# Kernel optimization log

Hardware: AMD Instinct MI355X
Metric: run time of the kernel (lower is better)

## Reference

```python
import jax, jax.numpy as jnp
import numpy as np

ISO = 0.0
DIM = 64
# MC corner numbering: 0..7 around the cube, main diagonal corner0=(0,0,0) -> corner6=(1,1,1)
OFF = [(0,0,0),(1,0,0),(1,1,0),(0,1,0),(0,0,1),(1,0,1),(1,1,1),(0,1,1)]
# 6-tetrahedra decomposition of a voxel around the 0-6 diagonal
TETS = np.array([[0,1,2,6],[0,2,3,6],[0,3,7,6],[0,7,4,6],[0,4,5,6],[0,5,1,6]], dtype=np.int32)
# tet edges: e0=(0,1) e1=(0,2) e2=(0,3) e3=(1,2) e4=(1,3) e5=(2,3)
EDGE_A = np.array([0,0,0,1,1,2], dtype=np.int32)
EDGE_B = np.array([1,2,3,2,3,3], dtype=np.int32)
# marching-tetrahedra case table: case = bitmask of (value > iso) per tet corner;
# each row lists up to 2 triangles as tet-edge ids, -1 = unused slot
TRI_TABLE = np.array([
    [-1,-1,-1,-1,-1,-1],
    [ 0, 1, 2,-1,-1,-1],
    [ 0, 4, 3,-1,-1,-1],
    [ 1, 2, 4, 1, 4, 3],
    [ 1, 3, 5,-1,-1,-1],
    [ 0, 3, 5, 0, 5, 2],
    [ 0, 4, 5, 0, 5, 1],
    [ 2, 4, 5,-1,-1,-1],
    [ 2, 5, 4,-1,-1,-1],
    [ 0, 5, 4, 0, 1, 5],
    [ 0, 5, 3, 0, 2, 5],
    [ 1, 5, 3,-1,-1,-1],
    [ 1, 4, 2, 1, 3, 4],
    [ 0, 3, 4,-1,-1,-1],
    [ 0, 2, 1,-1,-1,-1],
    [-1,-1,-1,-1,-1,-1]], dtype=np.int32)


def _mc(grid, deform, iso):
    X, Y, Z = grid.shape
    # pad scalar field with iso+1 (outside), deform with 0 -- mirrors DiffMC.forward
    Gp = jnp.pad(grid, 1, constant_values=iso + 1.0)
    Dp = jnp.pad(deform, ((1,1),(1,1),(1,1),(0,0)))
    ax = [jnp.arange(s, dtype=grid.dtype) for s in (X+2, Y+2, Z+2)]
    coords = jnp.stack(jnp.meshgrid(*ax, indexing='ij'), axis=-1)  # [X+2,Y+2,Z+2,3]
    P = coords + Dp                                                 # deformed grid-point positions
    Vx, Vy, Vz = X+1, Y+1, Z+1                                      # number of voxels per axis
    Vc = jnp.stack([Gp[dx:dx+Vx, dy:dy+Vy, dz:dz+Vz] for dx,dy,dz in OFF], axis=-1).reshape(-1, 8)
    Pc = jnp.stack([P[dx:dx+Vx, dy:dy+Vy, dz:dz+Vz] for dx,dy,dz in OFF], axis=-2).reshape(-1, 8, 3)
    tv = Vc[:, TETS].reshape(-1, 4)        # [M,4] tet corner values, M = 6*Vx*Vy*Vz
    tp = Pc[:, TETS].reshape(-1, 4, 3)     # [M,4,3] tet corner positions
    M = tv.shape[0]
    code = ((tv > iso).astype(jnp.int32) * jnp.array([1, 2, 4, 8], dtype=jnp.int32)).sum(-1)
    tri = jnp.asarray(TRI_TABLE)[code]     # [M,6] edge ids (2 triangle slots)
    valid = tri >= 0
    e = jnp.where(valid, tri, 0)
    a = jnp.asarray(EDGE_A)[e]
    b = jnp.asarray(EDGE_B)[e]
    va = jnp.take_along_axis(tv, a, axis=1)
    vb = jnp.take_along_axis(tv, b, axis=1)
    a3 = jnp.broadcast_to(a[:, :, None], (M, 6, 3))
    b3 = jnp.broadcast_to(b[:, :, None], (M, 6, 3))
    pa = jnp.take_along_axis(tp, a3, axis=1)
    pb = jnp.take_along_axis(tp, b3, axis=1)
    den = vb - va
    t = (iso - va) / jnp.where(jnp.abs(den) > 1e-8, den, 1.0)
    t = jnp.clip(t, 0.0, 1.0)[..., None]
    pos = pa + t * (pb - pa)               # edge-interpolated surface vertices [M,6,3]
    scale = jnp.array([X-1, Y-1, Z-1], dtype=grid.dtype)
    verts = ((pos - 1.0) / scale) * valid[..., None].astype(grid.dtype)  # undo pad, normalize to [0,1]
    verts = verts.reshape(-1, 3, 3)        # [2*M triangles, 3 corners, xyz]
    mask = valid.reshape(-1, 3)[:, 0]      # triangle validity (all 3 slots set together)
    return verts, mask


def setup_inputs() -> dict:
    key = jax.random.key(0)
    k1, k2 = jax.random.split(key)
    grid = jax.random.normal(k1, (DIM, DIM, DIM), dtype=jnp.float32)
    deform = 0.3 * jax.random.normal(k2, (DIM, DIM, DIM, 3), dtype=jnp.float32)
    return {"grid": grid, "deform": deform}


def reference(grid, deform):
    verts, mask = _mc(grid, deform, ISO)
    tris = jnp.arange(verts.shape[0] * 3, dtype=jnp.int32).reshape(-1, 3)
    return verts, tris, mask
```

## Files before the change

### kernel.cpp

```cpp
#include <hip/hip_runtime.h>
#include <stdint.h>

#define DIM   64
#define VPA   65
#define NVOX  (VPA*VPA*VPA)
#define NTET  (6*NVOX)
#define TRIS_OFF_F  29659500
#define MASK_OFF_F  39546000
#define NTPB 256

__constant__ unsigned int c_TRIP[16] = {
    0xFFFFFFu,
    0xFFF210u,
    0xFFF340u,
    0x341421u,
    0xFFF531u,
    0x250530u,
    0x150540u,
    0xFFF542u,
    0xFFF452u,
    0x510450u,
    0x520350u,
    0xFFF351u,
    0x431241u,
    0xFFF430u,
    0xFFF120u,
    0xFFFFFFu
};
__constant__ unsigned short c_TETP[6] = {
    0x6210u, 0x6320u, 0x6730u, 0x6470u, 0x6540u, 0x6150u
};
#define EA_PACK 0x211000u
#define EB_PACK 0x332321u
#define OFFX_MASK 0x66u
#define OFFY_MASK 0xCCu
#define OFFZ_MASK 0xF0u

__global__ __launch_bounds__(256) void mc_kernel(
    const float* __restrict__ grid,
    const float* __restrict__ deform,
    float* __restrict__ out)
{
    __shared__ __align__(16) float  ldsv[NTPB * 18];
    __shared__ __align__(16) float2 ldsm[NTPB];

    const int tid  = threadIdx.x;
    const int base = blockIdx.x * NTPB;
    const int m    = base + tid;
    const int nv   = min(NTPB, NTET - base);
    const bool full = (nv == NTPB);

    if (m < NTET) {
        int v = m / 6;
        int t = m - v * 6;
        int iz = v % VPA;
        int tmp = v / VPA;
        int iy = tmp % VPA;
        int ix = tmp / VPA;

        float tv[4];
        float tpx[4], tpy[4], tpz[4];
        unsigned int tet = c_TETP[t];
        #pragma unroll
        for (int c = 0; c < 4; ++c) {
            unsigned int corner = (tet >> (4 * c)) & 0xFu;
            int px = ix + (int)((OFFX_MASK >> corner) & 1u);
            int py = iy + (int)((OFFY_MASK >> corner) & 1u);
            int pz = iz + (int)((OFFZ_MASK >> corner) & 1u);
            bool interior = ((unsigned)(px - 1) < (unsigned)DIM) &
                            ((unsigned)(py - 1) < (unsigned)DIM) &
                            ((unsigned)(pz - 1) < (unsigned)DIM);
            float val = 1.0f;
            float dx = 0.f, dy = 0.f, dz = 0.f;
            if (interior) {
                int gi = ((px - 1) * DIM + (py - 1)) * DIM + (pz - 1);
                val = grid[gi];
                const float* d = deform + 3 * (size_t)gi;
                dx = d[0]; dy = d[1]; dz = d[2];
            }
            tv[c]  = val;
            tpx[c] = (float)px + dx;
            tpy[c] = (float)py + dy;
            tpz[c] = (float)pz + dz;
        }

        int code = (tv[0] > 0.f ? 1 : 0) | (tv[1] > 0.f ? 2 : 0) |
                   (tv[2] > 0.f ? 4 : 0) | (tv[3] > 0.f ? 8 : 0);
        unsigned int tri = c_TRIP[code];

        float verts[18];
        bool mask0 = false, mask1 = false;
        #pragma unroll
        for (int s = 0; s < 6; ++s) {
            unsigned int e4 = (tri >> (4 * s)) & 0xFu;
            bool valid = (e4 != 0xFu);
            unsigned int e = valid ? e4 : 0u;
            if (s == 0) mask0 = valid;
            if (s == 3) mask1 = valid;
            int a = (int)((EA_PACK >> (4 * e)) & 0xFu);
            int b = (int)((EB_PACK >> (4 * e)) & 0xFu);
            float va = tv[a], vb = tv[b];
            float den = vb - va;
            float dsafe = (fabsf(den) > 1e-8f) ? den : 1.0f;
            float tt = (0.0f - va) / dsafe;
            tt = fminf(fmaxf(tt, 0.0f), 1.0f);
            float vm = valid ? (1.0f / 63.0f) : 0.0f;
            float px = tpx[a] + tt * (tpx[b] - tpx[a]);
            float py = tpy[a] + tt * (tpy[b] - tpy[a]);
            float pz = tpz[a] + tt * (tpz[b] - tpz[a]);
            verts[s * 3 + 0] = (px - 1.0f) * vm;
            verts[s * 3 + 1] = (py - 1.0f) * vm;
            verts[s * 3 + 2] = (pz - 1.0f) * vm;
        }

        #pragma unroll
        for (int s2 = 0; s2 < 9; ++s2)
            *reinterpret_cast<float2*>(&ldsv[tid * 18 + 2 * s2]) =
                make_float2(verts[2 * s2], verts[2 * s2 + 1]);
        ldsm[tid] = make_float2(mask0 ? 1.0f : 0.0f, mask1 ? 1.0f : 0.0f);
    }

    {
        float* ot = out + (size_t)TRIS_OFF_F + (size_t)base * 6;
        float fb = (float)(6 * base);
        if (full) {
            float4* ot4 = reinterpret_cast<float4*>(ot);
            float v0 = fb + (float)(4 * tid);
            ot4[tid] = make_float4(v0, v0 + 1.f, v0 + 2.f, v0 + 3.f);
            if (tid < 128) {
                float v1 = fb + (float)(4 * (NTPB + tid));
                ot4[NTPB + tid] = make_float4(v1, v1 + 1.f, v1 + 2.f, v1 + 3.f);
            }
        } else {
            for (int p = tid; p < nv * 6; p += NTPB)
                ot[p] = fb + (float)p;
        }
    }

    __syncthreads();

    if (full) {
        const float4* lv4 = reinterpret_cast<const float4*>(ldsv);
        float4* ov4 = reinterpret_cast<float4*>(out + (size_t)base * 18);
        #pragma unroll
        for (int k = 0; k < 4; ++k)
            ov4[k * NTPB + tid] = lv4[k * NTPB + tid];
        if (tid < 128)
            ov4[4 * NTPB + tid] = lv4[4 * NTPB + tid];

        float4* om4 = reinterpret_cast<float4*>(out + (size_t)MASK_OFF_F + (size_t)base * 2);
        if (tid < 128)
            om4[tid] = reinterpret_cast<const float4*>(ldsm)[tid];
    } else {
        float* ov = out + (size_t)base * 18;
        for (int p = tid; p < nv * 18; p += NTPB)
            ov[p] = ldsv[p];
        float2* om = reinterpret_cast<float2*>(out + (size_t)MASK_OFF_F + (size_t)base * 2);
        if (tid < nv)
            om[tid] = ldsm[tid];
    }
}

extern "C" void kernel_launch(void* const* d_in, const int* in_sizes, int n_in,
                              void* d_out, int out_size, void* d_ws, size_t ws_size,
                              hipStream_t stream) {
    const float* grid   = (const float*)d_in[0];
    const float* deform = (const float*)d_in[1];
    float* out = (float*)d_out;

    int blocks = (NTET + NTPB - 1) / NTPB;
    mc_kernel<<<blocks, NTPB, 0, stream>>>(grid, deform, out);
}
```

Baseline: 35.79 us.

## Use grid-stride persistent blocks and per-wavefront LDS staging without block barrier

Replaces the one-block-per-256-tets launch with a fixed 2048-block grid-stride loop. It also removes the __syncthreads by having each 64-lane wavefront write out only its own slice of the LDS staging buffer. The aim is to cut block launch overhead and barrier stalls. The risk is an LDS race: no wave barrier or fence is used, and the next loop iteration may overwrite LDS before the reads finish, so correctness relies on wavefront lockstep. Fewer blocks may also limit latency hiding.

```diff
diff --git a/kernel.cpp b/kernel.cpp
--- a/kernel.cpp
+++ b/kernel.cpp
@@ -8,6 +8,8 @@
 #define TRIS_OFF_F  29659500
 #define MASK_OFF_F  39546000
 #define NTPB 256
+#define NBLK 2048
+#define NGEN ((NTET + NTPB - 1) / NTPB)
 
 __constant__ unsigned int c_TRIP[16] = {
     0xFFFFFFu,
@@ -44,120 +46,123 @@
     __shared__ __align__(16) float  ldsv[NTPB * 18];
     __shared__ __align__(16) float2 ldsm[NTPB];
 
-    const int tid  = threadIdx.x;
-    const int base = blockIdx.x * NTPB;
-    const int m    = base + tid;
-    const int nv   = min(NTPB, NTET - base);
-    const bool full = (nv == NTPB);
+    const int tid = threadIdx.x;
+    const int wv  = tid >> 6;
+    const int ln  = tid & 63;
 
-    if (m < NTET) {
-        int v = m / 6;
-        int t = m - v * 6;
-        int iz = v % VPA;
-        int tmp = v / VPA;
-        int iy = tmp % VPA;
-        int ix = tmp / VPA;
+    for (int gen = blockIdx.x; gen < NGEN; gen += NBLK) {
+        const int base = gen * NTPB;
+        const int m    = base + tid;
+        const int nv   = min(NTPB, NTET - base);
+        const bool full = (nv == NTPB);
 
-        float tv[4];
-        float tpx[4], tpy[4], tpz[4];
-        unsigned int tet = c_TETP[t];
-        #pragma unroll
-        for (int c = 0; c < 4; ++c) {
-            unsigned int corner = (tet >> (4 * c)) & 0xFu;
-            int px = ix + (int)((OFFX_MASK >> corner) & 1u);
-            int py = iy + (int)((OFFY_MASK >> corner) & 1u);
-            int pz = iz + (int)((OFFZ_MASK >> corner) & 1u);
-            bool interior = ((unsigned)(px - 1) < (unsigned)DIM) &
-                            ((unsigned)(py - 1) < (unsigned)DIM) &
-                            ((unsigned)(pz - 1) < (unsigned)DIM);
-            float val = 1.0f;
-            float dx = 0.f, dy = 0.f, dz = 0.f;
-            if (interior) {
-                int gi = ((px - 1) * DIM + (py - 1)) * DIM + (pz - 1);
-                val = grid[gi];
-                const float* d = deform + 3 * (size_t)gi;
-                dx = d[0]; dy = d[1]; dz = d[2];
+        if (m < NTET) {
+            int v = m / 6;
+            int t = m - v * 6;
+            int iz = v % VPA;
+            int tmp = v / VPA;
+            int iy = tmp % VPA;
+            int ix = tmp / VPA;
+
+            float tv[4];
+            float tpx[4], tpy[4], tpz[4];
+            unsigned int tet = c_TETP[t];
+            #pragma unroll
+            for (int c = 0; c < 4; ++c) {
+                unsigned int corner = (tet >> (4 * c)) & 0xFu;
+                int px = ix + (int)((OFFX_MASK >> corner) & 1u);
+                int py = iy + (int)((OFFY_MASK >> corner) & 1u);
+                int pz = iz + (int)((OFFZ_MASK >> corner) & 1u);
+                bool interior = ((unsigned)(px - 1) < (unsigned)DIM) &
+                                ((unsigned)(py - 1) < (unsigned)DIM) &
+                                ((unsigned)(pz - 1) < (unsigned)DIM);
+                float val = 1.0f;
+                float dx = 0.f, dy = 0.f, dz = 0.f;
+                if (interior) {
+                    int gi = ((px - 1) * DIM + (py - 1)) * DIM + (pz - 1);
+                    val = grid[gi];
+                    const float* d = deform + 3 * (size_t)gi;
+                    dx = d[0]; dy = d[1]; dz = d[2];
+                }
+                tv[c]  = val;
+                tpx[c] = (float)px + dx;
+                tpy[c] = (float)py + dy;
+                tpz[c] = (float)pz + dz;
             }
-            tv[c]  = val;
-            tpx[c] = (float)px + dx;
-            tpy[c] = (float)py + dy;
-            tpz[c] = (float)pz + dz;
+
+            int code = (tv[0] > 0.f ? 1 : 0) | (tv[1] > 0.f ? 2 : 0) |
+                       (tv[2] > 0.f ? 4 : 0) | (tv[3] > 0.f ? 8 : 0);
+            unsigned int tri = c_TRIP[code];
+
+            float verts[18];
+            bool mask0 = false, mask1 = false;
+            #pragma unroll
+            for (int s = 0; s < 6; ++s) {
+                unsigned int e4 = (tri >> (4 * s)) & 0xFu;
+                bool valid = (e4 != 0xFu);
+                unsigned int e = valid ? e4 : 0u;
+                if (s == 0) mask0 = valid;
+                if (s == 3) mask1 = valid;
+                int a = (int)((EA_PACK >> (4 * e)) & 0xFu);
+                int b = (int)((EB_PACK >> (4 * e)) & 0xFu);
+                float va = tv[a], vb = tv[b];
+                float den = vb - va;
+                float dsafe = (fabsf(den) > 1e-8f) ? den : 1.0f;
+                float tt = (0.0f - va) / dsafe;
+                tt = fminf(fmaxf(tt, 0.0f), 1.0f);
+                float vm = valid ? (1.0f / 63.0f) : 0.0f;
+                float px = tpx[a] + tt * (tpx[b] - tpx[a]);
+                float py = tpy[a] + tt * (tpy[b] - tpy[a]);
+                float pz = tpz[a] + tt * (tpz[b] - tpz[a]);
+                verts[s * 3 + 0] = (px - 1.0f) * vm;
+                verts[s * 3 + 1] = (py - 1.0f) * vm;
+                verts[s * 3 + 2] = (pz - 1.0f) * vm;
+            }
+
+            #pragma unroll
+            for (int s2 = 0; s2 < 9; ++s2)
+                *reinterpret_cast<float2*>(&ldsv[tid * 18 + 2 * s2]) =
+                    make_float2(verts[2 * s2], verts[2 * s2 + 1]);
+            ldsm[tid] = make_float2(mask0 ? 1.0f : 0.0f, mask1 ? 1.0f : 0.0f);
         }
 
-        int code = (tv[0] > 0.f ? 1 : 0) | (tv[1] > 0.f ? 2 : 0) |
-                   (tv[2] > 0.f ? 4 : 0) | (tv[3] > 0.f ? 8 : 0);
-        unsigned int tri = c_TRIP[code];
+        const int wbase = base + wv * 64;
 
-        float verts[18];
-        bool mask0 = false, mask1 = false;
-        #pragma unroll
-        for (int s = 0; s < 6; ++s) {
-            unsigned int e4 = (tri >> (4 * s)) & 0xFu;
-            bool valid = (e4 != 0xFu);
-            unsigned int e = valid ? e4 : 0u;
-            if (s == 0) mask0 = valid;
-            if (s == 3) mask1 = valid;
-            int a = (int)((EA_PACK >> (4 * e)) & 0xFu);
-            int b = (int)((EB_PACK >> (4 * e)) & 0xFu);
-            float va = tv[a], vb = tv[b];
-            float den = vb - va;
-            float dsafe = (fabsf(den) > 1e-8f) ? den : 1.0f;
-            float tt = (0.0f - va) / dsafe;
-            tt = fminf(fmaxf(tt, 0.0f), 1.0f);
-            float vm = valid ? (1.0f / 63.0f) : 0.0f;
-            float px = tpx[a] + tt * (tpx[b] - tpx[a]);
-            float py = tpy[a] + tt * (tpy[b] - tpy[a]);
-            float pz = tpz[a] + tt * (tpz[b] - tpz[a]);
-            verts[s * 3 + 0] = (px - 1.0f) * vm;
-            verts[s * 3 + 1] = (py - 1.0f) * vm;
-            verts[s * 3 + 2] = (pz - 1.0f) * vm;
+        if (full) {
+            const float4* lv4 = reinterpret_cast<const float4*>(ldsv + wv * 1152);
+            float4* ov4 = reinterpret_cast<float4*>(out + (size_t)wbase * 18);
+            #pragma unroll
+            for (int k = 0; k < 4; ++k)
+                ov4[k * 64 + ln] = lv4[k * 64 + ln];
+            if (ln < 32)
+                ov4[256 + ln] = lv4[256 + ln];
+
+            float4* ot4 = reinterpret_cast<float4*>(out + (size_t)TRIS_OFF_F + (size_t)wbase * 6);
+            float fb = (float)(wbase * 6);
+            {
+                float v0 = fb + (float)(4 * ln);
+                ot4[ln] = make_float4(v0, v0 + 1.f, v0 + 2.f, v0 + 3.f);
+                if (ln < 32) {
+                    float v1 = fb + (float)(4 * (64 + ln));
+                    ot4[64 + ln] = make_float4(v1, v1 + 1.f, v1 + 2.f, v1 + 3.f);
+                }
+            }
+
+            float4* om4 = reinterpret_cast<float4*>(out + (size_t)MASK_OFF_F + (size_t)wbase * 2);
+            if (ln < 32)
+                om4[ln] = reinterpret_cast<const float4*>(ldsm + wv * 64)[ln];
+        } else {
+            int nvw = nv - wv * 64;
+            nvw = nvw < 0 ? 0 : (nvw > 64 ? 64 : nvw);
+            const float* lsrc = ldsv + wv * 1152;
+            float* ov = out + (size_t)wbase * 18;
+            for (int p = ln; p < nvw * 18; p += 64) ov[p] = lsrc[p];
+            float* ot = out + (size_t)TRIS_OFF_F + (size_t)wbase * 6;
+            float fb = (float)(wbase * 6);
+            for (int p = ln; p < nvw * 6; p += 64) ot[p] = fb + (float)p;
+            float2* om = reinterpret_cast<float2*>(out + (size_t)MASK_OFF_F) + wbase;
+            if (ln < nvw) om[ln] = ldsm[wv * 64 + ln];
         }
-
-        #pragma unroll
-        for (int s2 = 0; s2 < 9; ++s2)
-            *reinterpret_cast<float2*>(&ldsv[tid * 18 + 2 * s2]) =
-                make_float2(verts[2 * s2], verts[2 * s2 + 1]);
-        ldsm[tid] = make_float2(mask0 ? 1.0f : 0.0f, mask1 ? 1.0f : 0.0f);
-    }
-
-    {
-        float* ot = out + (size_t)TRIS_OFF_F + (size_t)base * 6;
-        float fb = (float)(6 * base);
-        if (full) {
-            float4* ot4 = reinterpret_cast<float4*>(ot);
-            float v0 = fb + (float)(4 * tid);
-            ot4[tid] = make_float4(v0, v0 + 1.f, v0 + 2.f, v0 + 3.f);
-            if (tid < 128) {
-                float v1 = fb + (float)(4 * (NTPB + tid));
-                ot4[NTPB + tid] = make_float4(v1, v1 + 1.f, v1 + 2.f, v1 + 3.f);
-            }
-        } else {
-            for (int p = tid; p < nv * 6; p += NTPB)
-                ot[p] = fb + (float)p;
-        }
-    }
-
-    __syncthreads();
-
-    if (full) {
-        const float4* lv4 = reinterpret_cast<const float4*>(ldsv);
-        float4* ov4 = reinterpret_cast<float4*>(out + (size_t)base * 18);
-        #pragma unroll
-        for (int k = 0; k < 4; ++k)
-            ov4[k * NTPB + tid] = lv4[k * NTPB + tid];
-        if (tid < 128)
-            ov4[4 * NTPB + tid] = lv4[4 * NTPB + tid];
-
-        float4* om4 = reinterpret_cast<float4*>(out + (size_t)MASK_OFF_F + (size_t)base * 2);
-        if (tid < 128)
-            om4[tid] = reinterpret_cast<const float4*>(ldsm)[tid];
-    } else {
-        float* ov = out + (size_t)base * 18;
-        for (int p = tid; p < nv * 18; p += NTPB)
-            ov[p] = ldsv[p];
-        float2* om = reinterpret_cast<float2*>(out + (size_t)MASK_OFF_F + (size_t)base * 2);
-        if (tid < nv)
-            om[tid] = ldsm[tid];
     }
 }
 
@@ -168,6 +173,5 @@
     const float* deform = (const float*)d_in[1];
     float* out = (float*)d_out;
 
-    int blocks = (NTET + NTPB - 1) / NTPB;
-    mc_kernel<<<blocks, NTPB, 0, stream>>>(grid, deform, out);
+    mc_kernel<<<NBLK, NTPB, 0, stream>>>(grid, deform, out);
 }
```

Result: slower. 37.68 us (+5.3%).
